# Optimization experiments

Measured on AMD Instinct MI355X. Metric: run time of the kernel, lower is better.

Reference implementation:

```python
import jax, jax.numpy as jnp
from jax import lax
import numpy as np

H = W = 768
N_BOXES = 512
C1, C2 = 32, 64
POOL = 5
NUM_CLASSES = 4
BN_EPS = 1e-5


def setup_inputs() -> dict:
    key = jax.random.key(0)
    ks = jax.random.split(key, 20)
    image = jax.random.normal(ks[0], (1, 3, H, W), jnp.float32)
    # valid boxes: xmax>xmin, ymax>ymin, inside [0, W)
    xmin = jax.random.randint(ks[1], (N_BOXES,), 0, W - 256)
    ymin = jax.random.randint(ks[2], (N_BOXES,), 0, H - 256)
    bw = jax.random.randint(ks[3], (N_BOXES,), 8, 256)
    bh = jax.random.randint(ks[4], (N_BOXES,), 8, 256)
    boxes = jnp.stack([xmin, ymin, xmin + bw, ymin + bh], axis=1).astype(jnp.int32)
    conv1_w = jax.random.normal(ks[5], (C1, 3, 3, 3), jnp.float32) * 0.1
    conv1_b = jax.random.normal(ks[6], (C1,), jnp.float32) * 0.01
    bn1_g = 1.0 + 0.1 * jax.random.normal(ks[7], (C1,), jnp.float32)
    bn1_b = 0.1 * jax.random.normal(ks[8], (C1,), jnp.float32)
    bn1_m = 0.1 * jax.random.normal(ks[9], (C1,), jnp.float32)
    bn1_v = jax.random.uniform(ks[10], (C1,), jnp.float32, 0.5, 1.5)
    conv2_w = jax.random.normal(ks[11], (C2, C1, 3, 3), jnp.float32) * 0.05
    conv2_b = jax.random.normal(ks[12], (C2,), jnp.float32) * 0.01
    bn2_g = 1.0 + 0.1 * jax.random.normal(ks[13], (C2,), jnp.float32)
    bn2_b = 0.1 * jax.random.normal(ks[14], (C2,), jnp.float32)
    bn2_m = 0.1 * jax.random.normal(ks[15], (C2,), jnp.float32)
    bn2_v = jax.random.uniform(ks[16], (C2,), jnp.float32, 0.5, 1.5)
    fc1_w = jax.random.normal(ks[17], (128, C2 * POOL * POOL), jnp.float32) * 0.02
    fc1_b = jnp.zeros((128,), jnp.float32)
    fc2_w = jax.random.normal(ks[18], (NUM_CLASSES, 128), jnp.float32) * 0.05
    fc2_b = jnp.zeros((NUM_CLASSES,), jnp.float32)
    return dict(image=image, boxes=boxes,
                conv1_w=conv1_w, conv1_b=conv1_b, bn1_g=bn1_g, bn1_b=bn1_b, bn1_m=bn1_m, bn1_v=bn1_v,
                conv2_w=conv2_w, conv2_b=conv2_b, bn2_g=bn2_g, bn2_b=bn2_b, bn2_m=bn2_m, bn2_v=bn2_v,
                fc1_w=fc1_w, fc1_b=fc1_b, fc2_w=fc2_w, fc2_b=fc2_b)


def _conv(x, w, b):
    y = lax.conv_general_dilated(x, w, (1, 1), ((1, 1), (1, 1)),
                                 dimension_numbers=("NCHW", "OIHW", "NCHW"))
    return y + b[None, :, None, None]


def _bn(x, g, b, m, v):
    scale = g / jnp.sqrt(v + BN_EPS)
    return x * scale[None, :, None, None] + (b - m * scale)[None, :, None, None]


def _forward(image, boxes, conv1_w, conv1_b, bn1_g, bn1_b, bn1_m, bn1_v,
             conv2_w, conv2_b, bn2_g, bn2_b, bn2_m, bn2_v,
             fc1_w, fc1_b, fc2_w, fc2_b):
    # backbone: Conv -> ReLU -> BN (order as in source), twice
    x = _bn(jax.nn.relu(_conv(image, conv1_w, conv1_b)), bn1_g, bn1_b, bn1_m, bn1_v)
    x = _bn(jax.nn.relu(_conv(x, conv2_w, conv2_b)), bn2_g, bn2_b, bn2_m, bn2_v)
    feat = x[0]  # [C2, H, W], batch assumed 1 as in the per-box slicing loop
    # integral image for exact adaptive-avg-pool over integer index rectangles
    integ = jnp.pad(feat, ((0, 0), (1, 0), (1, 0))).cumsum(1).cumsum(2)  # [C2,H+1,W+1]
    xmin, ymin, xmax, ymax = boxes[:, 0], boxes[:, 1], boxes[:, 2], boxes[:, 3]
    bh = ymax - ymin
    bw = xmax - xmin
    i = jnp.arange(POOL)
    # AdaptiveAvgPool2d bin edges: start=floor(i*L/5), end=ceil((i+1)*L/5)
    y0 = ymin[:, None] + (i * bh[:, None]) // POOL            # [N,5]
    y1 = ymin[:, None] + ((i + 1) * bh[:, None] + POOL - 1) // POOL
    x0 = xmin[:, None] + (i * bw[:, None]) // POOL
    x1 = xmin[:, None] + ((i + 1) * bw[:, None] + POOL - 1) // POOL

    def rect(ys, xs):  # [C2, N, 5, 5]
        return integ[:, ys[:, :, None], xs[:, None, :]]

    s = rect(y1, x1) - rect(y0, x1) - rect(y1, x0) + rect(y0, x0)
    area = ((y1 - y0)[:, :, None] * (x1 - x0)[:, None, :]).astype(feat.dtype)  # [N,5,5]
    pooled = s / area[None]                                    # [C2,N,5,5]
    flat = pooled.transpose(1, 0, 2, 3).reshape(boxes.shape[0], -1)  # [N, C2*25]
    h1 = jax.nn.relu(flat @ fc1_w.T + fc1_b)  # dropout is identity in eval
    return h1 @ fc2_w.T + fc2_b               # [N, num_classes]


def reference(image, boxes, conv1_w, conv1_b, bn1_g, bn1_b, bn1_m, bn1_v,
              conv2_w, conv2_b, bn2_g, bn2_b, bn2_m, bn2_v,
              fc1_w, fc1_b, fc2_w, fc2_b):
    return _forward(image, boxes, conv1_w, conv1_b, bn1_g, bn1_b, bn1_m, bn1_v,
                    conv2_w, conv2_b, bn2_g, bn2_b, bn2_m, bn2_v,
                    fc1_w, fc1_b, fc2_w, fc2_b)
```

## Files before the change

kernel.cpp:

```cpp
#include <hip/hip_runtime.h>
#include <hip/hip_bf16.h>

#define HH 768
#define WW 768
#define HWSZ (HH*WW)
#define BN_EPS 1e-5f
#define SEG 8
#define NSEG 96

typedef __attribute__((ext_vector_type(8))) short bf16x8;
typedef __attribute__((ext_vector_type(4))) float f32x4;

__device__ __forceinline__ float bf2f(unsigned short u) {
  union { unsigned int i; float f; } v; v.i = ((unsigned int)u) << 16; return v.f;
}
__device__ __forceinline__ unsigned short f2bf(float f) {
  union { float f; unsigned int i; } v; v.f = f;
  unsigned int x = v.i;
  return (unsigned short)((x + 0x7fffu + ((x >> 16) & 1u)) >> 16);
}
__device__ __forceinline__ float ldf(const void* p, int i, int flag) {
  return flag ? bf2f(((const unsigned short*)p)[i]) : ((const float*)p)[i];
}

#define DPP_ADD(v, CTRL) do {                                              \
    union { float f; int i; } _u; _u.f = (v);                              \
    int _t = __builtin_amdgcn_update_dpp(0, _u.i, (CTRL), 0xf, 0xf, true); \
    union { int i; float f; } _w; _w.i = _t;                               \
    (v) += _w.f;                                                           \
  } while (0)
__device__ __forceinline__ float row_prefix16(float v) {
  DPP_ADD(v, 0x111);
  DPP_ADD(v, 0x112);
  DPP_ADD(v, 0x114);
  DPP_ADD(v, 0x118);
  return v;
}

__device__ __forceinline__ int detect_flag(const void* v1) {
  const unsigned short* v1raw = (const unsigned short*)v1;
  int ok = 1;
  #pragma unroll
  for (int j = 0; j < 4; ++j) {
    unsigned short u = v1raw[2*j];
    if (u < 0x3E00u || u > 0x4040u) ok = 0;
  }
  return ok;
}

__global__ void k_prep(const void* __restrict__ c1b,
                       const void* __restrict__ g1, const void* __restrict__ b1,
                       const void* __restrict__ m1, const void* __restrict__ v1,
                       const void* __restrict__ c2b, const void* __restrict__ g2,
                       const void* __restrict__ b2, const void* __restrict__ m2,
                       const void* __restrict__ v2, const void* __restrict__ w1,
                       const void* __restrict__ fb1, const void* __restrict__ fw2,
                       const void* __restrict__ fb2, const void* __restrict__ w2,
                       const void* __restrict__ fw1,
                       int* __restrict__ flagp, float* __restrict__ cst,
                       unsigned short* __restrict__ A2, unsigned short* __restrict__ A1,
                       unsigned short* __restrict__ w1c)
{
  int flag = detect_flag(v1);
  int tid = threadIdx.x, bid = blockIdx.x;
  int gid = bid * 256 + tid;

  if (bid == 0) {
    if (tid == 0) *flagp = flag;
    float* bias1 = cst + 864;
    float* sc1   = cst + 896;
    float* sh1   = cst + 928;
    float* bias2 = cst + 960;
    float* sc2   = cst + 1024;
    float* sh2   = cst + 1088;
    float* fb1c  = cst + 1152;
    float* w2c   = cst + 1280;
    float* fb2c  = cst + 1792;
    if (tid < 32) {
      float s = ldf(g1, tid, flag) * rsqrtf(ldf(v1, tid, flag) + BN_EPS);
      sc1[tid] = s;
      sh1[tid] = ldf(b1, tid, flag) - ldf(m1, tid, flag) * s;
      bias1[tid] = ldf(c1b, tid, flag);
    }
    if (tid < 64) {
      float s = ldf(g2, tid, flag) * rsqrtf(ldf(v2, tid, flag) + BN_EPS);
      sc2[tid] = s;
      sh2[tid] = ldf(b2, tid, flag) - ldf(m2, tid, flag) * s;
      bias2[tid] = ldf(c2b, tid, flag);
    }
    if (tid < 128) fb1c[tid] = ldf(fb1, tid, flag);
    if (tid < 4)   fb2c[tid] = ldf(fb2, tid, flag);
    for (int i = tid; i < 512; i += 256) w2c[i] = ldf(fw2, i, flag);
  }
  if (gid < 80*288) {
    int o = gid / 288, k = gid % 288, tap = k >> 5, ci = k & 31;
    A2[gid] = (o < 64) ? f2bf(ldf(w2, (o*32 + ci)*9 + tap, flag)) : (unsigned short)0;
  }
  if (gid < 32*64) {
    int o = gid >> 6, k = gid & 63, tap = k >> 2, ci = k & 3;
    A1[gid] = (tap < 9 && ci < 3) ? f2bf(ldf(w1, o*27 + ci*9 + tap, flag))
                                  : (unsigned short)0;
  }
  for (int i = gid; i < 128*1600; i += 128*256) {
    int t = i / 1600, r = i % 1600, cell = r >> 6, c = r & 63;
    w1c[i] = f2bf(ldf(fw1, t*1600 + c*25 + cell, flag));
  }
}

__global__ __launch_bounds__(256) void k_conv12t(const void* __restrict__ img,
    const int* __restrict__ flagp, const unsigned short* __restrict__ A1,
    const unsigned short* __restrict__ A2, const float* __restrict__ cst,
    float* __restrict__ T)
{
  const float* bias1 = cst + 864;
  const float* sc1   = cst + 896;
  const float* sh1   = cst + 928;
  const float* bias2 = cst + 960;
  const float* sc2   = cst + 1024;
  const float* sh2   = cst + 1088;
  __shared__ unsigned short ftile[10 * 34 * 40];
  __shared__ unsigned short itile[12 * 36 * 4];
  int flag = *flagp;
  int tid = threadIdx.x;
  int xb = blockIdx.x, ys = blockIdx.y;
  int x0 = xb * 32, ybase = ys * SEG;

  for (int idx = tid; idx < 12*36; idx += 256) {
    int r = idx / 36, p = idx % 36;
    int gy = ybase - 2 + r, gx = x0 - 2 + p;
    unsigned short e0 = 0, e1 = 0, e2 = 0;
    if (gy >= 0 && gy < HH && gx >= 0 && gx < WW) {
      e0 = f2bf(ldf(img, 0*HWSZ + gy*WW + gx, flag));
      e1 = f2bf(ldf(img, 1*HWSZ + gy*WW + gx, flag));
      e2 = f2bf(ldf(img, 2*HWSZ + gy*WW + gx, flag));
    }
    ushort4 pk; pk.x = e0; pk.y = e1; pk.z = e2; pk.w = 0;
    *(ushort4*)(itile + idx*4) = pk;
  }

  int w = tid >> 6, lane = tid & 63, quad = lane >> 4, l16 = lane & 15;

  bf16x8 a1f[2][2];
  #pragma unroll
  for (int mt = 0; mt < 2; ++mt)
    #pragma unroll
    for (int kt = 0; kt < 2; ++kt)
      a1f[mt][kt] = *(const bf16x8*)(A1 + (mt*16 + l16)*64 + kt*32 + quad*8);
  int t0 = 2*quad, t1 = 2*quad + 1;
  int ky0 = t0/3, kx0 = t0%3, ky1 = t1/3, kx1 = t1%3;

  int m = w * 16 + l16;
  bf16x8 afrag[9];
  #pragma unroll
  for (int t = 0; t < 9; ++t)
    afrag[t] = *(const bf16x8*)(A2 + m*288 + t*32 + quad*8);
  float bs[4], scv[4], shv[4];
  #pragma unroll
  for (int r = 0; r < 4; ++r) {
    int c = w*16 + quad*4 + r;
    bs[r] = bias2[c]; scv[r] = sc2[c]; shv[r] = sh2[c];
  }
  __syncthreads();

  for (int u = w; u < 30; u += 4) {
    int r = u / 3, nt = u % 3;
    int pxb = nt*16 + l16;
    int pp = (pxb <= 33) ? pxb : 33;
    union { uint2 q[2]; bf16x8 v; } b0;
    b0.q[0] = *(const uint2*)(itile + ((r + ky0)*36 + pp + kx0)*4);
    b0.q[1] = *(const uint2*)(itile + ((r + ky1)*36 + pp + kx1)*4);
    union { uint2 q[2]; bf16x8 v; } b1v;
    b1v.q[0] = *(const uint2*)(itile + ((r + 2)*36 + pp + 2)*4);
    b1v.q[1] = make_uint2(0u, 0u);
    f32x4 acc[2];
    acc[0] = (f32x4){0.f,0.f,0.f,0.f};
    acc[1] = (f32x4){0.f,0.f,0.f,0.f};
    #pragma unroll
    for (int mt = 0; mt < 2; ++mt) {
      acc[mt] = __builtin_amdgcn_mfma_f32_16x16x32_bf16(a1f[mt][0], b0.v, acc[mt], 0, 0, 0);
      acc[mt] = __builtin_amdgcn_mfma_f32_16x16x32_bf16(a1f[mt][1], b1v.v, acc[mt], 0, 0, 0);
    }
    int py = ybase - 1 + r, gx = x0 - 1 + pxb;
    int inside = (py >= 0 && py < HH && gx >= 0 && gx < WW);
    if (pxb < 34) {
      #pragma unroll
      for (int mt = 0; mt < 2; ++mt) {
        int cb = mt*16 + quad*4;
        ushort4 pk;
        if (inside) {
          pk.x = f2bf(fmaxf(acc[mt][0] + bias1[cb+0], 0.f) * sc1[cb+0] + sh1[cb+0]);
          pk.y = f2bf(fmaxf(acc[mt][1] + bias1[cb+1], 0.f) * sc1[cb+1] + sh1[cb+1]);
          pk.z = f2bf(fmaxf(acc[mt][2] + bias1[cb+2], 0.f) * sc1[cb+2] + sh1[cb+2]);
          pk.w = f2bf(fmaxf(acc[mt][3] + bias1[cb+3], 0.f) * sc1[cb+3] + sh1[cb+3]);
        } else {
          pk.x = pk.y = pk.z = pk.w = 0;
        }
        *(ushort4*)(ftile + (r*34 + pxb)*40 + cb) = pk;
      }
    }
  }
  __syncthreads();

  f32x4 ys0 = (f32x4){0.f,0.f,0.f,0.f};
  f32x4 ys1 = (f32x4){0.f,0.f,0.f,0.f};
  int cbase = w*16 + quad*4;
  for (int dy = 0; dy < SEG; ++dy) {
    int y = ybase + dy;
    f32x4 acc[2];
    acc[0] = (f32x4){0.f,0.f,0.f,0.f};
    acc[1] = (f32x4){0.f,0.f,0.f,0.f};
    #pragma unroll
    for (int t = 0; t < 9; ++t) {
      int ky = t / 3, kx = t % 3;
      #pragma unroll
      for (int i = 0; i < 2; ++i) {
        int px = i*16 + l16 + kx;
        bf16x8 b = *(const bf16x8*)(ftile + ((dy + ky)*34 + px)*40 + quad*8);
        acc[i] = __builtin_amdgcn_mfma_f32_16x16x32_bf16(afrag[t], b, acc[i], 0, 0, 0);
      }
    }
    #pragma unroll
    for (int r = 0; r < 4; ++r) {
      float v0 = fmaxf(acc[0][r] + bs[r], 0.f) * scv[r] + shv[r];
      float v1 = fmaxf(acc[1][r] + bs[r], 0.f) * scv[r] + shv[r];
      v0 = row_prefix16(v0);
      v1 = row_prefix16(v1);
      v1 += __shfl(v0, 15, 16);
      ys0[r] += v0;
      ys1[r] += v1;
    }
    *(f32x4*)(T + ((size_t)(y*WW + x0 + l16))*64 + cbase)      = ys0;
    *(f32x4*)(T + ((size_t)(y*WW + x0 + 16 + l16))*64 + cbase) = ys1;
  }
}

__global__ __launch_bounds__(256) void k_cgen(const float* __restrict__ T,
                                              float* __restrict__ C)
{
  __shared__ float Sp[NSEG*24];
  int cc = blockIdx.x, tid = threadIdx.x;
  for (int idx = tid; idx < NSEG*24; idx += 256) {
    int i = idx / 24, j = idx % 24;
    Sp[idx] = T[((size_t)((i*SEG + SEG-1)*WW + j*32 + 31))*64 + cc];
  }
  __syncthreads();
  if (tid < 24) {
    float run = 0.f;
    for (int i = 0; i < NSEG; ++i) { run += Sp[i*24 + tid]; Sp[i*24 + tid] = run; }
  }
  __syncthreads();
  if (tid < NSEG) {
    float run = 0.f;
    #pragma unroll
    for (int j = 0; j < 24; ++j) { run += Sp[tid*24 + j]; Sp[tid*24 + j] = run; }
  }
  __syncthreads();
  for (int idx = tid; idx < NSEG*24; idx += 256)
    C[((size_t)idx)*64 + cc] = Sp[idx];
}

__global__ __launch_bounds__(256) void k_ab(const float* __restrict__ T,
    const float* __restrict__ C, float* __restrict__ A, float* __restrict__ Bp)
{
  __shared__ float gtot[4][64];
  int part = blockIdx.y, tid = threadIdx.x;
  int c = tid & 63, g = tid >> 6;
  if (part == 0) {
    int y = blockIdx.x;
    float vals[6];
    float run = 0.f;
    #pragma unroll
    for (int jj = 0; jj < 6; ++jj) {
      int j = g*6 + jj;
      run += T[((size_t)(y*WW + j*32 + 31))*64 + c];
      vals[jj] = run;
    }
    gtot[g][c] = run;
    __syncthreads();
    float off = 0.f;
    for (int gg = 0; gg < g; ++gg) off += gtot[gg][c];
    #pragma unroll
    for (int jj = 0; jj < 6; ++jj)
      A[((size_t)(y*24 + g*6 + jj))*64 + c] = vals[jj] + off;
  } else {
    int x = blockIdx.x;
    int j = x >> 5;
    float vals[24];
    float run = 0.f;
    #pragma unroll 4
    for (int ii = 0; ii < 24; ++ii) {
      int i = g*24 + ii;
      run += T[((size_t)((i*SEG + SEG-1)*WW + x))*64 + c];
      vals[ii] = run;
    }
    gtot[g][c] = run;
    __syncthreads();
    float off = 0.f;
    for (int gg = 0; gg < g; ++gg) off += gtot[gg][c];
    #pragma unroll 4
    for (int ii = 0; ii < 24; ++ii) {
      int i = g*24 + ii;
      float cj = (j > 0) ? C[((size_t)(i*24 + (j-1)))*64 + c] : 0.f;
      Bp[((size_t)(i*WW + x))*64 + c] = vals[ii] + off + cj;
    }
  }
}

__device__ __forceinline__ float icorner(const float* __restrict__ T,
    const float* __restrict__ A, const float* __restrict__ Bp,
    int c, int yy, int xx)
{
  int i = yy >> 3, j = xx >> 5;
  float v = T[((size_t)(yy*WW + xx))*64 + c];
  if (j > 0) v += A[((size_t)(yy*24 + (j-1)))*64 + c];
  if (i > 0) v += Bp[((size_t)((i-1)*WW + xx))*64 + c];
  return v;
}

__global__ __launch_bounds__(256) void k_roi3(const float* __restrict__ T,
    const float* __restrict__ A, const float* __restrict__ Bp,
    const int* __restrict__ boxes, unsigned short* __restrict__ flat)
{
  int b = blockIdx.x;
  int xmin = boxes[b*4 + 0], ymin = boxes[b*4 + 1];
  int xmax = boxes[b*4 + 2], ymax = boxes[b*4 + 3];
  int bh = ymax - ymin, bw = xmax - xmin;
  for (int idx = threadIdx.x; idx < 1600; idx += 256) {
    int c = idx & 63, cell = idx >> 6, i = cell / 5, j = cell % 5;
    int y0 = ymin + (i*bh)/5,  y1 = ymin + ((i+1)*bh + 4)/5;
    int x0 = xmin + (j*bw)/5,  x1 = xmin + ((j+1)*bw + 4)/5;
    float s = icorner(T, A, Bp, c, y1-1, x1-1);
    if (y0 > 0)           s -= icorner(T, A, Bp, c, y0-1, x1-1);
    if (x0 > 0)           s -= icorner(T, A, Bp, c, y1-1, x0-1);
    if (y0 > 0 && x0 > 0) s += icorner(T, A, Bp, c, y0-1, x0-1);
    float area = (float)((y1 - y0) * (x1 - x0));
    flat[b*1600 + cell*64 + c] = f2bf(s / area);
  }
}

__global__ __launch_bounds__(256) void k_fcm(const unsigned short* __restrict__ flat,
    const unsigned short* __restrict__ w1c, const float* __restrict__ cst,
    const int* __restrict__ flagp, void* __restrict__ out)
{
  const float* fb1c = cst + 1152;
  const float* w2c  = cst + 1280;
  const float* fb2c = cst + 1792;
  __shared__ unsigned short sflat[16 * 1608];
  __shared__ float hbuf[16 * 132];
  int tid = threadIdx.x;
  int b0 = blockIdx.x * 16;
  for (int ii = tid; ii < 3200; ii += 256) {
    int bi = ii / 200, ch = ii % 200;
    *(uint4*)(sflat + bi*1608 + ch*8) = *(const uint4*)(flat + (b0 + bi)*1600 + ch*8);
  }
  __syncthreads();
  int w = tid >> 6, lane = tid & 63, quad = lane >> 4, l16 = lane & 15;
  f32x4 acc[2];
  acc[0] = (f32x4){0.f,0.f,0.f,0.f};
  acc[1] = (f32x4){0.f,0.f,0.f,0.f};
  for (int kt = 0; kt < 50; ++kt) {
    bf16x8 b = *(const bf16x8*)(sflat + l16*1608 + kt*32 + quad*8);
    #pragma unroll
    for (int mt = 0; mt < 2; ++mt) {
      bf16x8 a = *(const bf16x8*)(w1c + ((w*2 + mt)*16 + l16)*1600 + kt*32 + quad*8);
      acc[mt] = __builtin_amdgcn_mfma_f32_16x16x32_bf16(a, b, acc[mt], 0, 0, 0);
    }
  }
  #pragma unroll
  for (int mt = 0; mt < 2; ++mt) {
    #pragma unroll
    for (int r = 0; r < 4; ++r) {
      int h = (w*2 + mt)*16 + quad*4 + r;
      hbuf[l16*132 + h] = fmaxf(acc[mt][r] + fb1c[h], 0.f);
    }
  }
  __syncthreads();
  if (tid < 64) {
    int bi = tid >> 2, o = tid & 3;
    float a2 = fb2c[o];
    for (int k = 0; k < 128; ++k) a2 += hbuf[bi*132 + k] * w2c[o*128 + k];
    if (*flagp) ((unsigned short*)out)[(b0 + bi)*4 + o] = f2bf(a2);
    else        ((float*)out)[(b0 + bi)*4 + o] = a2;
  }
}

__global__ __launch_bounds__(256) void k_conv1m(const void* __restrict__ img,
    const int* __restrict__ flagp, const unsigned short* __restrict__ A1,
    const float* __restrict__ cst, unsigned short* __restrict__ feat1)
{
  const float* bias1 = cst + 864;
  const float* sc1   = cst + 896;
  const float* sh1   = cst + 928;
  int flag = *flagp;
  __shared__ unsigned short tile[18 * 34 * 4];
  int tid = threadIdx.x;
  int x0 = blockIdx.x * 32, ybase = blockIdx.y * 16;
  for (int idx = tid; idx < 18*34; idx += 256) {
    int r = idx / 34, p = idx % 34;
    int gy = ybase - 1 + r, gx = x0 - 1 + p;
    unsigned short e0 = 0, e1 = 0, e2 = 0;
    if (gy >= 0 && gy < HH && gx >= 0 && gx < WW) {
      e0 = f2bf(ldf(img, 0*HWSZ + gy*WW + gx, flag));
      e1 = f2bf(ldf(img, 1*HWSZ + gy*WW + gx, flag));
      e2 = f2bf(ldf(img, 2*HWSZ + gy*WW + gx, flag));
    }
    ushort4 pk; pk.x = e0; pk.y = e1; pk.z = e2; pk.w = 0;
    *(ushort4*)(tile + idx*4) = pk;
  }
  int w = tid >> 6, lane = tid & 63, quad = lane >> 4, l16 = lane & 15;
  bf16x8 a1f[2][2];
  #pragma unroll
  for (int mt = 0; mt < 2; ++mt)
    #pragma unroll
    for (int kt = 0; kt < 2; ++kt)
      a1f[mt][kt] = *(const bf16x8*)(A1 + (mt*16 + l16)*64 + kt*32 + quad*8);
  int t0 = 2*quad, t1 = 2*quad + 1;
  int ky0 = t0/3, kx0 = t0%3, ky1 = t1/3, kx1 = t1%3;
  __syncthreads();
  for (int dyw = 0; dyw < 4; ++dyw) {
    int dy = dyw*4 + w;
    int y = ybase + dy;
    f32x4 acc[2][2];
    #pragma unroll
    for (int mt = 0; mt < 2; ++mt)
      #pragma unroll
      for (int i = 0; i < 2; ++i)
        acc[mt][i] = (f32x4){0.f,0.f,0.f,0.f};
    #pragma unroll
    for (int i = 0; i < 2; ++i) {
      int pxb = i*16 + l16;
      union { uint2 q[2]; bf16x8 v; } b0;
      b0.q[0] = *(const uint2*)(tile + ((dy + ky0)*34 + pxb + kx0)*4);
      b0.q[1] = *(const uint2*)(tile + ((dy + ky1)*34 + pxb + kx1)*4);
      union { uint2 q[2]; bf16x8 v; } b1v;
      b1v.q[0] = *(const uint2*)(tile + ((dy + 2)*34 + pxb + 2)*4);
      b1v.q[1] = make_uint2(0u, 0u);
      #pragma unroll
      for (int mt = 0; mt < 2; ++mt) {
        acc[mt][i] = __builtin_amdgcn_mfma_f32_16x16x32_bf16(a1f[mt][0], b0.v, acc[mt][i], 0, 0, 0);
        acc[mt][i] = __builtin_amdgcn_mfma_f32_16x16x32_bf16(a1f[mt][1], b1v.v, acc[mt][i], 0, 0, 0);
      }
    }
    #pragma unroll
    for (int mt = 0; mt < 2; ++mt) {
      int cb = mt*16 + quad*4;
      #pragma unroll
      for (int i = 0; i < 2; ++i) {
        int px = x0 + i*16 + l16;
        ushort4 pk;
        pk.x = f2bf(fmaxf(acc[mt][i][0] + bias1[cb+0], 0.f) * sc1[cb+0] + sh1[cb+0]);
        pk.y = f2bf(fmaxf(acc[mt][i][1] + bias1[cb+1], 0.f) * sc1[cb+1] + sh1[cb+1]);
        pk.z = f2bf(fmaxf(acc[mt][i][2] + bias1[cb+2], 0.f) * sc1[cb+2] + sh1[cb+2]);
        pk.w = f2bf(fmaxf(acc[mt][i][3] + bias1[cb+3], 0.f) * sc1[cb+3] + sh1[cb+3]);
        *(ushort4*)(feat1 + ((size_t)(y*WW + px))*32 + cb) = pk;
      }
    }
  }
}
__global__ __launch_bounds__(256) void k_conv2_c16(const unsigned short* __restrict__ feat1,
    const unsigned short* __restrict__ A2, const float* __restrict__ cst,
    float* __restrict__ chunk, int c0, int cnw)
{
  const float* bias2 = cst + 960;
  const float* sc2   = cst + 1024;
  const float* sh2   = cst + 1088;
  __shared__ unsigned short tile[3 * 130 * 40];
  int tid = threadIdx.x;
  int y = blockIdx.y, x0 = blockIdx.x * 128;
  for (int idx = tid; idx < 3*130*4; idx += 256) {
    int q = idx & 3, p = (idx >> 2) % 130, r = idx / 520;
    int gy = y - 1 + r, gx = x0 - 1 + p;
    uint4 val = make_uint4(0u, 0u, 0u, 0u);
    if (gy >= 0 && gy < HH && gx >= 0 && gx < WW)
      val = *(const uint4*)(feat1 + (gy*WW + gx)*32 + q*8);
    *(uint4*)(tile + (r*130 + p)*40 + q*8) = val;
  }
  __syncthreads();
  int w = tid >> 6, lane = tid & 63, quad = lane >> 4, l16 = lane & 15;
  int m = c0 + l16;
  f32x4 acc[2];
  acc[0] = (f32x4){0.f,0.f,0.f,0.f};
  acc[1] = (f32x4){0.f,0.f,0.f,0.f};
  #pragma unroll
  for (int t = 0; t < 9; ++t) {
    int ky = t / 3, kx = t % 3;
    bf16x8 a = *(const bf16x8*)(A2 + m*288 + t*32 + quad*8);
    #pragma unroll
    for (int i = 0; i < 2; ++i) {
      int px = w*32 + i*16 + l16 + kx;
      bf16x8 b = *(const bf16x8*)(tile + (ky*130 + px)*40 + quad*8);
      acc[i] = __builtin_amdgcn_mfma_f32_16x16x32_bf16(a, b, acc[i], 0, 0, 0);
    }
  }
  #pragma unroll
  for (int r = 0; r < 4; ++r) {
    int cl = quad*4 + r;
    if (cl < cnw) {
      int c = c0 + cl;
      float bsv = bias2[c], s = sc2[c], sh = sh2[c];
      float* dst = chunk + cl*HWSZ + y*WW;
      #pragma unroll
      for (int i = 0; i < 2; ++i) {
        float v = fmaxf(acc[i][r] + bsv, 0.f) * s + sh;
        dst[x0 + w*32 + i*16 + l16] = v;
      }
    }
  }
}
__global__ __launch_bounds__(256) void k_csy(float* __restrict__ buf) {
  int t = blockIdx.x * 256 + threadIdx.x;
  int c = t / WW, x = t % WW;
  float* p = buf + c*HWSZ + x;
  float run = 0.f;
  for (int yb = 0; yb < HH; yb += 16) {
    float v[16];
    #pragma unroll
    for (int j = 0; j < 16; ++j) v[j] = p[(yb + j) * WW];
    #pragma unroll
    for (int j = 0; j < 16; ++j) { run += v[j]; v[j] = run; }
    #pragma unroll
    for (int j = 0; j < 16; ++j) p[(yb + j) * WW] = v[j];
  }
}
__global__ __launch_bounds__(256) void k_csx(float* __restrict__ buf) {
  int row = blockIdx.x * 4 + (threadIdx.x >> 6);
  int lane = threadIdx.x & 63;
  float* p = buf + (long)row * WW;
  float carry = 0.f;
  for (int ch = 0; ch < 12; ++ch) {
    float v = p[ch*64 + lane];
    #pragma unroll
    for (int off = 1; off < 64; off <<= 1) {
      float t = __shfl_up(v, off);
      v = (lane >= off) ? v + t : v;
    }
    v += carry;
    p[ch*64 + lane] = v;
    carry = __shfl(v, 63);
  }
}
__global__ __launch_bounds__(256) void k_roi(const float* __restrict__ integ,
    const int* __restrict__ boxes, unsigned short* __restrict__ flat, int c0, int cn)
{
  int b = blockIdx.x;
  int xmin = boxes[b*4 + 0], ymin = boxes[b*4 + 1];
  int xmax = boxes[b*4 + 2], ymax = boxes[b*4 + 3];
  int bh = ymax - ymin, bw = xmax - xmin;
  for (int idx = threadIdx.x; idx < cn*25; idx += 256) {
    int cl = idx / 25, cell = idx % 25, i = cell / 5, j = cell % 5;
    int y0 = ymin + (i*bh)/5,      y1 = ymin + ((i+1)*bh + 4)/5;
    int x0 = xmin + (j*bw)/5,      x1 = xmin + ((j+1)*bw + 4)/5;
    const float* I = integ + cl*HWSZ;
    float a  = I[(y1-1)*WW + (x1-1)];
    float bl = (y0 > 0) ? I[(y0-1)*WW + (x1-1)] : 0.f;
    float cr = (x0 > 0) ? I[(y1-1)*WW + (x0-1)] : 0.f;
    float d  = (y0 > 0 && x0 > 0) ? I[(y0-1)*WW + (x0-1)] : 0.f;
    float s = a - bl - cr + d;
    float area = (float)((y1 - y0) * (x1 - x0));
    flat[b*1600 + cell*64 + (c0 + cl)] = f2bf(s / area);
  }
}

extern "C" void kernel_launch(void* const* d_in, const int* in_sizes, int n_in,
                              void* d_out, int out_size, void* d_ws, size_t ws_size,
                              hipStream_t stream) {
  const void* img = d_in[0];
  const int* boxes = (const int*)d_in[1];
  const void* c1w = d_in[2];  const void* c1b = d_in[3];
  const void* g1  = d_in[4];  const void* b1  = d_in[5];
  const void* m1  = d_in[6];  const void* v1  = d_in[7];
  const void* c2w = d_in[8];  const void* c2b = d_in[9];
  const void* g2  = d_in[10]; const void* b2  = d_in[11];
  const void* m2  = d_in[12]; const void* v2  = d_in[13];
  const void* fw1 = d_in[14]; const void* fb1 = d_in[15];
  const void* fw2 = d_in[16]; const void* fb2 = d_in[17];

  char* ws = (char*)d_ws;
  unsigned short* A2 = (unsigned short*)ws;
  unsigned short* A1 = (unsigned short*)(ws + 46080);
  float* cst = (float*)(ws + 50176);
  int* flag = (int*)(ws + 57360);
  unsigned short* w1c  = (unsigned short*)(ws + 3592224);
  unsigned short* flat = (unsigned short*)(ws + 4001824);
  unsigned short* feat1 = (unsigned short*)(ws + 7278624);
  float* T = (float*)(ws + 45027360);
  float* Aarr = (float*)(ws + 7278624);
  float* Bparr = Aarr + (size_t)768*24*64;
  float* Carr = Bparr + (size_t)NSEG*768*64;

  const size_t base = 45027360;
  int cn;
  if      (ws_size >= base + 64ull*HWSZ*4) cn = 64;
  else if (ws_size >= base + 16ull*HWSZ*4) cn = 16;
  else if (ws_size >= base +  8ull*HWSZ*4) cn = 8;
  else if (ws_size >= base +  4ull*HWSZ*4) cn = 4;
  else if (ws_size >= base +  2ull*HWSZ*4) cn = 2;
  else                                     cn = 1;

  hipLaunchKernelGGL(k_prep, dim3(128), dim3(256), 0, stream,
                     c1b, g1, b1, m1, v1, c2b, g2, b2, m2, v2, c1w,
                     fb1, fw2, fb2, c2w, fw1, flag, cst, A2, A1, w1c);

  if (cn == 64) {
    hipLaunchKernelGGL(k_conv12t, dim3(24, NSEG), dim3(256), 0, stream,
                       img, flag, A1, A2, cst, T);
    hipLaunchKernelGGL(k_cgen, dim3(64), dim3(256), 0, stream, T, Carr);
    hipLaunchKernelGGL(k_ab, dim3(768, 2), dim3(256), 0, stream, T, Carr, Aarr, Bparr);
    hipLaunchKernelGGL(k_roi3, dim3(512), dim3(256), 0, stream,
                       T, Aarr, Bparr, boxes, flat);
  } else {
    hipLaunchKernelGGL(k_conv1m, dim3(24, 48), dim3(256), 0, stream,
                       img, flag, A1, cst, feat1);
    for (int c0 = 0; c0 < 64; c0 += cn) {
      hipLaunchKernelGGL(k_conv2_c16, dim3(6, 768), dim3(256), 0, stream,
                         feat1, A2, cst, T, c0, cn);
      hipLaunchKernelGGL(k_csy, dim3(cn*3), dim3(256), 0, stream, T);
      hipLaunchKernelGGL(k_csx, dim3(cn*192), dim3(256), 0, stream, T);
      hipLaunchKernelGGL(k_roi, dim3(512), dim3(256), 0, stream, T, boxes, flat, c0, cn);
    }
  }
  hipLaunchKernelGGL(k_fcm, dim3(32), dim3(256), 0, stream, flat, w1c, cst, flag,
                     d_out);
}
```

Baseline: 210.2 us.

## Write prefix-sum tensor only at positions needed by ROI corner lookups

```diff
diff --git a/kernel.cpp b/kernel.cpp
--- a/kernel.cpp
+++ b/kernel.cpp
@@ -59,11 +59,13 @@
                        const void* __restrict__ fw1,
                        int* __restrict__ flagp, float* __restrict__ cst,
                        unsigned short* __restrict__ A2, unsigned short* __restrict__ A1,
-                       unsigned short* __restrict__ w1c)
+                       unsigned short* __restrict__ w1c, unsigned int* __restrict__ mask)
 {
   int flag = detect_flag(v1);
   int tid = threadIdx.x, bid = blockIdx.x;
   int gid = bid * 256 + tid;
+
+  for (int i = gid; i < 768*24; i += 128*256) mask[i] = 0u;
 
   if (bid == 0) {
     if (tid == 0) *flagp = flag;
@@ -107,10 +109,28 @@
   }
 }
 
+__global__ __launch_bounds__(128) void k_mask(const int* __restrict__ boxes,
+                                              unsigned int* __restrict__ mask)
+{
+  int b = blockIdx.x, t = threadIdx.x;
+  if (t >= 100) return;
+  int a = t / 10, cix = t % 10;
+  int xmin = boxes[b*4 + 0], ymin = boxes[b*4 + 1];
+  int xmax = boxes[b*4 + 2], ymax = boxes[b*4 + 3];
+  int bh = ymax - ymin, bw = xmax - xmin;
+  int y, x;
+  if (a < 5) y = ymin + ((a+1)*bh + 4)/5 - 1;
+  else       y = ymin + ((a-5)*bh)/5 - 1;
+  if (cix < 5) x = xmin + ((cix+1)*bw + 4)/5 - 1;
+  else         x = xmin + ((cix-5)*bw)/5 - 1;
+  if (y >= 0 && x >= 0)
+    atomicOr(&mask[y*24 + (x >> 5)], 1u << (x & 31));
+}
+
 __global__ __launch_bounds__(256) void k_conv12t(const void* __restrict__ img,
     const int* __restrict__ flagp, const unsigned short* __restrict__ A1,
     const unsigned short* __restrict__ A2, const float* __restrict__ cst,
-    float* __restrict__ T)
+    const unsigned int* __restrict__ mask, float* __restrict__ T)
 {
   const float* bias1 = cst + 864;
   const float* sc1   = cst + 896;
@@ -229,8 +249,13 @@
       ys0[r] += v0;
       ys1[r] += v1;
     }
-    *(f32x4*)(T + ((size_t)(y*WW + x0 + l16))*64 + cbase)      = ys0;
-    *(f32x4*)(T + ((size_t)(y*WW + x0 + 16 + l16))*64 + cbase) = ys1;
+    unsigned int mw = mask[y*24 + xb];
+    int need0 = (dy == SEG-1) || ((mw >> l16) & 1u);
+    int need1 = (dy == SEG-1) || (l16 == 15) || ((mw >> (16 + l16)) & 1u);
+    if (need0)
+      *(f32x4*)(T + ((size_t)(y*WW + x0 + l16))*64 + cbase)      = ys0;
+    if (need1)
+      *(f32x4*)(T + ((size_t)(y*WW + x0 + 16 + l16))*64 + cbase) = ys1;
   }
 }
 
@@ -580,6 +605,7 @@
   unsigned short* A1 = (unsigned short*)(ws + 46080);
   float* cst = (float*)(ws + 50176);
   int* flag = (int*)(ws + 57360);
+  unsigned int* mask = (unsigned int*)(ws + 57376);
   unsigned short* w1c  = (unsigned short*)(ws + 3592224);
   unsigned short* flat = (unsigned short*)(ws + 4001824);
   unsigned short* feat1 = (unsigned short*)(ws + 7278624);
@@ -599,11 +625,12 @@
 
   hipLaunchKernelGGL(k_prep, dim3(128), dim3(256), 0, stream,
                      c1b, g1, b1, m1, v1, c2b, g2, b2, m2, v2, c1w,
-                     fb1, fw2, fb2, c2w, fw1, flag, cst, A2, A1, w1c);
+                     fb1, fw2, fb2, c2w, fw1, flag, cst, A2, A1, w1c, mask);
 
   if (cn == 64) {
+    hipLaunchKernelGGL(k_mask, dim3(512), dim3(128), 0, stream, boxes, mask);
     hipLaunchKernelGGL(k_conv12t, dim3(24, NSEG), dim3(256), 0, stream,
-                       img, flag, A1, A2, cst, T);
+                       img, flag, A1, A2, cst, mask, T);
     hipLaunchKernelGGL(k_cgen, dim3(64), dim3(256), 0, stream, T, Carr);
     hipLaunchKernelGGL(k_ab, dim3(768, 2), dim3(256), 0, stream, T, Carr, Aarr, Bparr);
     hipLaunchKernelGGL(k_roi3, dim3(512), dim3(256), 0, stream,
```

New measurement: 211.4 us. About the same (+0.5%).
